# Kernel optimization log

Measured on AMD Instinct MI355X. Metric: run time of the kernel, lower is better.

## Reference

```python
import jax, jax.numpy as jnp
import numpy as np

IN_DIM = 32768
CLASSES = 100
BATCH = 4096


def fast_sign(w):
    # forward: sign(w); backward: clamp(w, -1.3, 1.3) straight-through estimator
    clamped = jnp.clip(w, -1.3, 1.3)
    return jax.lax.stop_gradient(jnp.sign(w) - clamped) + clamped


def setup_inputs() -> dict:
    key = jax.random.key(0)
    kx, kw = jax.random.split(key)
    x = jax.random.normal(kx, (BATCH, IN_DIM), dtype=jnp.float32)
    W = jax.random.normal(kw, (CLASSES, IN_DIM), dtype=jnp.float32)
    return {"x": x, "W": W}


def reference(x, W):
    # BinaryLinear (bias=False) followed by 1/sqrt(in_dim) scaling
    scale = 1.0 / (IN_DIM ** 0.5)
    wb = fast_sign(W)                    # [classes, in_dim] in {-1, +1}
    return jnp.einsum('bk,ck->bc', x, wb) * scale
```

## Files before the change

kernel.cpp:

```cpp
#include <hip/hip_runtime.h>
#include <stdint.h>

#define IN_DIM 32768
#define CLASSES 100
#define BATCH 4096
#define NPAD 112
#define BK 32
#define MTILE 128
#define SPLITK 16
#define KCHUNK (IN_DIM / SPLITK)
#define NSTEP (KCHUNK / BK)
#define MBLOCKS (BATCH / MTILE)
#define WTILE_ELEMS (NPAD * BK)

typedef __attribute__((ext_vector_type(8))) short short8;
typedef __attribute__((ext_vector_type(4))) float floatx4;
typedef __attribute__((ext_vector_type(4))) uint32_t uintx4;

__device__ inline uint32_t f2bf(float f) {
  union { float f; uint32_t u; } v; v.f = f;
  uint32_t u = v.u;
  u += 0x7FFFu + ((u >> 16) & 1u);
  return u >> 16;
}
__device__ inline uint32_t pk(float a, float b) {
  return f2bf(a) | (f2bf(b) << 16);
}

__device__ inline void async_cp16(const void* g, void* l) {
  __builtin_amdgcn_global_load_lds(
      (const __attribute__((address_space(1))) uint32_t*)g,
      (__attribute__((address_space(3))) uint32_t*)l,
      16, 0, 0);
}

__global__ void pack_w_kernel(const float* __restrict__ W, short* __restrict__ wp) {
  int idx = blockIdx.x * 256 + threadIdx.x;
  int c = idx >> 15;
  int kg = idx & (IN_DIM - 1);
  short val = 0;
  if (c < CLASSES) {
    float w = W[((size_t)c << 15) + kg];
    val = (w > 0.0f) ? (short)0x3F80 : ((w < 0.0f) ? (short)0xBF80 : (short)0);
  }
  int kstep = kg >> 5;
  int rem = kg & 31;
  int kq = rem >> 3;
  int j = rem & 7;
  int nt = c >> 4;
  int n = c & 15;
  wp[(size_t)kstep * WTILE_ELEMS + nt * 512 + kq * 128 + n * 8 + j] = val;
}

__global__ __launch_bounds__(256, 2) void gemm_kernel(const float* __restrict__ x,
                                                      const short* __restrict__ wp,
                                                      float* __restrict__ out) {
  __shared__ __align__(16) short xlds[MTILE * BK];
  __shared__ __align__(16) short wlds[WTILE_ELEMS];

  const int tid = threadIdx.x;
  const int lane = tid & 63;
  const int w = tid >> 6;
  const int mb = blockIdx.x & (MBLOCKS - 1);
  const int ks = blockIdx.x >> 5;
  const int m_base = mb * MTILE;
  const int k0 = ks * KCHUNK;

  floatx4 acc[2][7];
#pragma unroll
  for (int i = 0; i < 2; ++i)
#pragma unroll
    for (int j = 0; j < 7; ++j) acc[i][j] = (floatx4)0.0f;

  const int row_l = tid >> 1;
  const int khalf = tid & 1;
  const float* xrow = x + (size_t)(m_base + row_l) * IN_DIM + k0 + khalf * 16;
  const int mg = row_l >> 4;
  const int nn = row_l & 15;
  uint32_t* xdst0 = (uint32_t*)&xlds[mg * 512 + (khalf * 2) * 128 + nn * 8];
  uint32_t* xdst1 = xdst0 + 64;

  const short8* xa = (const short8*)xlds;
  const short8* wb = (const short8*)wlds;

  for (int t = 0; t < NSTEP; ++t) {
    if (t) __syncthreads();

    const short* wsrc = wp + (size_t)(ks * NSTEP + t) * WTILE_ELEMS;
    async_cp16(wsrc + tid * 8, &wlds[tid * 8]);
    if (tid < 192)
      async_cp16(wsrc + (256 + tid) * 8, &wlds[(256 + tid) * 8]);

    const float* xp = xrow + t * BK;
    floatx4 f0 = *(const floatx4*)(xp);
    floatx4 f1 = *(const floatx4*)(xp + 4);
    floatx4 f2 = *(const floatx4*)(xp + 8);
    floatx4 f3 = *(const floatx4*)(xp + 12);
    uintx4 p0 = { pk(f0.x, f0.y), pk(f0.z, f0.w), pk(f1.x, f1.y), pk(f1.z, f1.w) };
    uintx4 p1 = { pk(f2.x, f2.y), pk(f2.z, f2.w), pk(f3.x, f3.y), pk(f3.z, f3.w) };
    *(uintx4*)xdst0 = p0;
    *(uintx4*)xdst1 = p1;

    __syncthreads();

    short8 a0 = xa[(2 * w) * 64 + lane];
    short8 a1 = xa[(2 * w + 1) * 64 + lane];
#pragma unroll
    for (int nt = 0; nt < 7; ++nt) {
      short8 b = wb[nt * 64 + lane];
      acc[0][nt] = __builtin_amdgcn_mfma_f32_16x16x32_bf16(a0, b, acc[0][nt], 0, 0, 0);
      acc[1][nt] = __builtin_amdgcn_mfma_f32_16x16x32_bf16(a1, b, acc[1][nt], 0, 0, 0);
    }
  }

  const float scale = 0.005524271728019903f;
  const int quad = lane >> 4;
  const int n16 = lane & 15;
#pragma unroll
  for (int mgi = 0; mgi < 2; ++mgi) {
    int row0 = m_base + w * 32 + mgi * 16 + quad * 4;
#pragma unroll
    for (int nt = 0; nt < 7; ++nt) {
      int col = nt * 16 + n16;
      if (col < CLASSES) {
#pragma unroll
        for (int r = 0; r < 4; ++r)
          atomicAdd(&out[(size_t)(row0 + r) * CLASSES + col], acc[mgi][nt][r] * scale);
      }
    }
  }
}

extern "C" void kernel_launch(void* const* d_in, const int* in_sizes, int n_in,
                              void* d_out, int out_size, void* d_ws, size_t ws_size,
                              hipStream_t stream) {
  const float* x = (const float*)d_in[0];
  const float* W = (const float*)d_in[1];
  float* out = (float*)d_out;
  short* wp = (short*)d_ws;

  hipMemsetAsync(d_out, 0, (size_t)BATCH * CLASSES * sizeof(float), stream);
  pack_w_kernel<<<(NPAD * IN_DIM) / 256, 256, 0, stream>>>(W, wp);
  gemm_kernel<<<MBLOCKS * SPLITK, 256, 0, stream>>>(x, wp, out);
}
```

Before: 765.2 us.

## Double-buffer W tiles, load x directly into registers, replace atomics with reduce

New measurement: 745.8 us. 1.03x faster.

```diff
diff --git a/kernel.cpp b/kernel.cpp
--- a/kernel.cpp
+++ b/kernel.cpp
@@ -6,16 +6,19 @@
 #define BATCH 4096
 #define NPAD 112
 #define BK 32
-#define MTILE 128
+#define MTILE 64
 #define SPLITK 16
 #define KCHUNK (IN_DIM / SPLITK)
 #define NSTEP (KCHUNK / BK)
 #define MBLOCKS (BATCH / MTILE)
 #define WTILE_ELEMS (NPAD * BK)
+#define NTILES (SPLITK * NSTEP)
+#define WP_ELEMS (NPAD * IN_DIM)
+#define PART_STRIDE (BATCH * NPAD)
+#define PART_OFF_BYTES (8u << 20)
 
 typedef __attribute__((ext_vector_type(8))) short short8;
 typedef __attribute__((ext_vector_type(4))) float floatx4;
-typedef __attribute__((ext_vector_type(4))) uint32_t uintx4;
 
 __device__ inline uint32_t f2bf(float f) {
   union { float f; uint32_t u; } v; v.f = f;
@@ -52,83 +55,85 @@
   wp[(size_t)kstep * WTILE_ELEMS + nt * 512 + kq * 128 + n * 8 + j] = val;
 }
 
-__global__ __launch_bounds__(256, 2) void gemm_kernel(const float* __restrict__ x,
+__global__ __launch_bounds__(256, 4) void gemm_kernel(const float* __restrict__ x,
                                                       const short* __restrict__ wp,
-                                                      float* __restrict__ out) {
-  __shared__ __align__(16) short xlds[MTILE * BK];
-  __shared__ __align__(16) short wlds[WTILE_ELEMS];
+                                                      float* __restrict__ part) {
+  __shared__ __align__(16) short wlds[2][WTILE_ELEMS];
 
   const int tid = threadIdx.x;
   const int lane = tid & 63;
   const int w = tid >> 6;
   const int mb = blockIdx.x & (MBLOCKS - 1);
-  const int ks = blockIdx.x >> 5;
+  const int ks = blockIdx.x >> 6;
   const int m_base = mb * MTILE;
-  const int k0 = ks * KCHUNK;
+  const int quad = lane >> 4;
 
-  floatx4 acc[2][7];
+  const float* xp = x + (size_t)(m_base + w * 16 + (lane & 15)) * IN_DIM
+                      + ks * KCHUNK + quad * 8;
+
+  floatx4 acc[7];
 #pragma unroll
-  for (int i = 0; i < 2; ++i)
-#pragma unroll
-    for (int j = 0; j < 7; ++j) acc[i][j] = (floatx4)0.0f;
+  for (int n = 0; n < 7; ++n) acc[n] = (floatx4)0.0f;
 
-  const int row_l = tid >> 1;
-  const int khalf = tid & 1;
-  const float* xrow = x + (size_t)(m_base + row_l) * IN_DIM + k0 + khalf * 16;
-  const int mg = row_l >> 4;
-  const int nn = row_l & 15;
-  uint32_t* xdst0 = (uint32_t*)&xlds[mg * 512 + (khalf * 2) * 128 + nn * 8];
-  uint32_t* xdst1 = xdst0 + 64;
-
-  const short8* xa = (const short8*)xlds;
-  const short8* wb = (const short8*)wlds;
+  {
+    const short* ws0 = wp + (size_t)(ks * NSTEP) * WTILE_ELEMS;
+    async_cp16(ws0 + tid * 8, &wlds[0][tid * 8]);
+    if (tid < 192)
+      async_cp16(ws0 + (256 + tid) * 8, &wlds[0][(256 + tid) * 8]);
+  }
+  floatx4 g0 = *(const floatx4*)xp;
+  floatx4 g1 = *(const floatx4*)(xp + 4);
 
   for (int t = 0; t < NSTEP; ++t) {
-    if (t) __syncthreads();
-
-    const short* wsrc = wp + (size_t)(ks * NSTEP + t) * WTILE_ELEMS;
-    async_cp16(wsrc + tid * 8, &wlds[tid * 8]);
-    if (tid < 192)
-      async_cp16(wsrc + (256 + tid) * 8, &wlds[(256 + tid) * 8]);
-
-    const float* xp = xrow + t * BK;
-    floatx4 f0 = *(const floatx4*)(xp);
-    floatx4 f1 = *(const floatx4*)(xp + 4);
-    floatx4 f2 = *(const floatx4*)(xp + 8);
-    floatx4 f3 = *(const floatx4*)(xp + 12);
-    uintx4 p0 = { pk(f0.x, f0.y), pk(f0.z, f0.w), pk(f1.x, f1.y), pk(f1.z, f1.w) };
-    uintx4 p1 = { pk(f2.x, f2.y), pk(f2.z, f2.w), pk(f3.x, f3.y), pk(f3.z, f3.w) };
-    *(uintx4*)xdst0 = p0;
-    *(uintx4*)xdst1 = p1;
-
     __syncthreads();
 
-    short8 a0 = xa[(2 * w) * 64 + lane];
-    short8 a1 = xa[(2 * w + 1) * 64 + lane];
+    int tile = ks * NSTEP + t + 1;
+    if (tile > NTILES - 1) tile = NTILES - 1;
+    const short* wsrc = wp + (size_t)tile * WTILE_ELEMS;
+    short* wdst = wlds[(t + 1) & 1];
+    async_cp16(wsrc + tid * 8, wdst + tid * 8);
+    if (tid < 192)
+      async_cp16(wsrc + (256 + tid) * 8, wdst + (256 + tid) * 8);
+
+    short8 a;
+    uint32_t* au = (uint32_t*)&a;
+    au[0] = pk(g0.x, g0.y); au[1] = pk(g0.z, g0.w);
+    au[2] = pk(g1.x, g1.y); au[3] = pk(g1.z, g1.w);
+
+    int tn = (t + 1 < NSTEP) ? t + 1 : 0;
+    const float* xn = xp + tn * BK;
+    g0 = *(const floatx4*)xn;
+    g1 = *(const floatx4*)(xn + 4);
+
+    const short8* wb = (const short8*)wlds[t & 1];
 #pragma unroll
-    for (int nt = 0; nt < 7; ++nt) {
-      short8 b = wb[nt * 64 + lane];
-      acc[0][nt] = __builtin_amdgcn_mfma_f32_16x16x32_bf16(a0, b, acc[0][nt], 0, 0, 0);
-      acc[1][nt] = __builtin_amdgcn_mfma_f32_16x16x32_bf16(a1, b, acc[1][nt], 0, 0, 0);
+    for (int n = 0; n < 7; ++n) {
+      short8 b = wb[n * 64 + lane];
+      acc[n] = __builtin_amdgcn_mfma_f32_16x16x32_bf16(a, b, acc[n], 0, 0, 0);
     }
   }
 
-  const float scale = 0.005524271728019903f;
-  const int quad = lane >> 4;
-  const int n16 = lane & 15;
+  float* pr = part + (size_t)ks * PART_STRIDE;
+  const int r0 = m_base + w * 16 + quad * 4;
+  const int c16 = lane & 15;
 #pragma unroll
-  for (int mgi = 0; mgi < 2; ++mgi) {
-    int row0 = m_base + w * 32 + mgi * 16 + quad * 4;
+  for (int n = 0; n < 7; ++n) {
+    int col = n * 16 + c16;
 #pragma unroll
-    for (int nt = 0; nt < 7; ++nt) {
-      int col = nt * 16 + n16;
-      if (col < CLASSES) {
+    for (int r = 0; r < 4; ++r)
+      pr[(size_t)(r0 + r) * NPAD + col] = acc[n][r];
+  }
+}
+
+__global__ void reduce_kernel(const float* __restrict__ part, float* __restrict__ out) {
+  int b = blockIdx.x;
+  int c = threadIdx.x;
+  if (c >= CLASSES) return;
+  const float* p = part + (size_t)b * NPAD + c;
+  float s = 0.0f;
 #pragma unroll
-        for (int r = 0; r < 4; ++r)
-          atomicAdd(&out[(size_t)(row0 + r) * CLASSES + col], acc[mgi][nt][r] * scale);
-      }
-    }
-  }
+  for (int ks = 0; ks < SPLITK; ++ks) s += p[(size_t)ks * PART_STRIDE];
+  out[(size_t)b * CLASSES + c] = s * 0.005524271728019903f;
 }
 
 extern "C" void kernel_launch(void* const* d_in, const int* in_sizes, int n_in,
@@ -138,8 +143,9 @@
   const float* W = (const float*)d_in[1];
   float* out = (float*)d_out;
   short* wp = (short*)d_ws;
+  float* part = (float*)((char*)d_ws + PART_OFF_BYTES);
 
-  hipMemsetAsync(d_out, 0, (size_t)BATCH * CLASSES * sizeof(float), stream);
-  pack_w_kernel<<<(NPAD * IN_DIM) / 256, 256, 0, stream>>>(W, wp);
-  gemm_kernel<<<MBLOCKS * SPLITK, 256, 0, stream>>>(x, wp, out);
+  pack_w_kernel<<<WP_ELEMS / 256, 256, 0, stream>>>(W, wp);
+  gemm_kernel<<<MBLOCKS * SPLITK, 256, 0, stream>>>(x, wp, part);
+  reduce_kernel<<<BATCH, 128, 0, stream>>>(part, out);
 }
```
